# Kernel optimization log

Measured on AMD Instinct MI355X. Metric: run time of the kernel, lower is better.

## Reference

```python
import jax, jax.numpy as jnp
import numpy as np

H = 512   # hidden_size
E = 256   # embedding_size
V = 32000 # vocab_size
L = 1024  # max_length (encoder seq len)
B = 64    # batch


def setup_inputs() -> dict:
    key = jax.random.key(0)
    ks = jax.random.split(key, 18)
    n = lambda i, shape, s=0.05: (jax.random.normal(ks[i], shape, dtype=jnp.float32) * s)
    return {
        "input": jax.random.randint(ks[0], (B, 1), 0, V),
        "last_output_context": n(1, (1, B, H), 1.0),
        "last_hidden": n(2, (1, B, H), 1.0),
        "last_cell_state": n(3, (1, B, H), 1.0),
        "encoder_outputs": n(4, (L, B, H), 1.0),
        "emb": n(5, (V, E)),
        "W_ih": n(6, (4 * H, E + H)),
        "W_hh": n(7, (4 * H, H)),
        "b_ih": n(8, (4 * H,)),
        "b_hh": n(9, (4 * H,)),
        "W_attn": n(10, (H, 2 * H)),
        "b_attn": n(11, (H,)),
        "beta": n(12, (H, 1), 1.0),
        "W_oc": n(13, (H, 2 * H)),
        "b_oc": n(14, (H,)),
        "W_out": n(15, (V, H)),
        "b_out": n(16, (V,)),
    }


def reference(input, last_output_context, last_hidden, last_cell_state,
              encoder_outputs, emb, W_ih, W_hh, b_ih, b_hh,
              W_attn, b_attn, beta, W_oc, b_oc, W_out, b_out):
    # embedding lookup: (B,1) -> (B,E)  (permute(1,0,2) then squeeze step dim)
    tok = emb[input[:, 0]]                                   # (B, E)
    x = jnp.concatenate([tok, last_output_context[0]], axis=1)  # (B, E+H)
    # single-step LSTM (PyTorch gate order i, f, g, o)
    gates = x @ W_ih.T + last_hidden[0] @ W_hh.T + b_ih + b_hh  # (B, 4H)
    i_g, f_g, g_g, o_g = jnp.split(gates, 4, axis=1)
    i_g = jax.nn.sigmoid(i_g)
    f_g = jax.nn.sigmoid(f_g)
    g_g = jnp.tanh(g_g)
    o_g = jax.nn.sigmoid(o_g)
    c = f_g * last_cell_state[0] + i_g * g_g                  # (B, H)
    h = o_g * jnp.tanh(c)                                     # (B, H) == rnn_output
    # additive attention, vectorized over the seq_len loop
    h_tiled = jnp.broadcast_to(h[None], (L, B, H))
    cat = jnp.concatenate([h_tiled, encoder_outputs], axis=-1)  # (L, B, 2H)
    energy = jnp.tanh(cat @ W_attn.T + b_attn) @ beta           # (L, B, 1)
    attn_w = jax.nn.softmax(energy[..., 0], axis=0)             # (L, B) softmax over seq
    # context = bmm(attn_weights, encoder_outputs)
    context = jnp.einsum('lb,lbh->bh', attn_w, encoder_outputs)  # (B, H)
    co = jnp.tanh(jnp.concatenate([h, context], axis=1) @ W_oc.T + b_oc)  # (B, H)
    output = jax.nn.log_softmax(co @ W_out.T + b_out, axis=1)    # (B, V)
    return output, co[None], h[None], c[None]
```

## Files before the change

kernel.cpp:

```cpp
#include <hip/hip_runtime.h>
#include <hip/hip_bf16.h>
#include <cstddef>

#define H   512
#define E   256
#define V   32000
#define L   1024
#define B   64
#define KX  768
#define M_TOT 65536

typedef __attribute__((ext_vector_type(8))) _Float16 half8v;
typedef __attribute__((ext_vector_type(4))) float f32x4;

__device__ __forceinline__ half8v cvt8(float4 x0, float4 x1) {
    union { half8v v; _Float16 u[8]; } hv;
    hv.u[0] = (_Float16)x0.x; hv.u[1] = (_Float16)x0.y;
    hv.u[2] = (_Float16)x0.z; hv.u[3] = (_Float16)x0.w;
    hv.u[4] = (_Float16)x1.x; hv.u[5] = (_Float16)x1.y;
    hv.u[6] = (_Float16)x1.z; hv.u[7] = (_Float16)x1.w;
    return hv.v;
}

__device__ __forceinline__ void glds16(const void* g, void* l) {
    __builtin_amdgcn_global_load_lds(
        (const __attribute__((address_space(1))) void*)g,
        (__attribute__((address_space(3))) void*)l, 16, 0, 0);
}

__global__ __launch_bounds__(256) void k_conv_w3(const float* __restrict__ W_attn,
                                                 unsigned short* __restrict__ WfB) {
    int u = blockIdx.x * 256 + threadIdx.x;
    int lane = u & 63;
    int rest = u >> 6;
    int kh = rest & 1, nf = (rest >> 1) & 3, wn = (rest >> 3) & 1;
    int kt2 = (rest >> 4) & 7, jt = rest >> 7;
    int j = jt * 128 + wn * 64 + nf * 16 + (lane & 15);
    int col = kt2 * 64 + kh * 32 + (lane >> 4) * 8;
    const float* src = &W_attn[(size_t)j * (2 * H) + H + col];
    float4 x0 = *reinterpret_cast<const float4*>(src);
    float4 x1 = *reinterpret_cast<const float4*>(src + 4);
    *reinterpret_cast<half8v*>(&WfB[(size_t)u * 8]) = cvt8(x0, x1);
}

__global__ __launch_bounds__(256) void k_build(const int* __restrict__ inp,
                                               const float* __restrict__ loc,
                                               const float* __restrict__ hprev,
                                               const float* __restrict__ emb,
                                               float* __restrict__ xprevT) {
    int gid = blockIdx.x * 256 + threadIdx.x;
    int k = gid >> 6, b = gid & 63;
    float v;
    if (k < 256)      v = emb[(size_t)inp[b] * E + k];
    else if (k < 768) v = loc[b * H + (k - 256)];
    else              v = hprev[b * H + (k - 768)];
    xprevT[gid] = v;
}

__global__ __launch_bounds__(256) void k_lstm(const float* __restrict__ W_ih,
                                              const float* __restrict__ W_hh,
                                              const float* __restrict__ b_ih,
                                              const float* __restrict__ b_hh,
                                              const float* __restrict__ xprevT,
                                              const float* __restrict__ cprev,
                                              float* __restrict__ h_out,
                                              float* __restrict__ c_out,
                                              float* __restrict__ hnewT) {
    int u = blockIdx.x;
    int w = threadIdx.x >> 6;
    int b = threadIdx.x & 63;
    int j = w * 512 + u;
    float a0 = 0.f, a1 = 0.f, a2 = 0.f, a3 = 0.f;
    const float* Wr = &W_ih[(size_t)j * KX];
    for (int k = 0; k < KX; k += 4) {
        float4 wv = *reinterpret_cast<const float4*>(&Wr[k]);
        a0 += wv.x * xprevT[(k + 0) * 64 + b];
        a1 += wv.y * xprevT[(k + 1) * 64 + b];
        a2 += wv.z * xprevT[(k + 2) * 64 + b];
        a3 += wv.w * xprevT[(k + 3) * 64 + b];
    }
    const float* Wr2 = &W_hh[(size_t)j * H];
    const float* hT = &xprevT[KX * 64];
    for (int k = 0; k < H; k += 4) {
        float4 wv = *reinterpret_cast<const float4*>(&Wr2[k]);
        a0 += wv.x * hT[(k + 0) * 64 + b];
        a1 += wv.y * hT[(k + 1) * 64 + b];
        a2 += wv.z * hT[(k + 2) * 64 + b];
        a3 += wv.w * hT[(k + 3) * 64 + b];
    }
    float acc = b_ih[j] + b_hh[j] + ((a0 + a1) + (a2 + a3));
    __shared__ float gs[4][64];
    gs[w][b] = acc;
    __syncthreads();
    if (threadIdx.x < 64) {
        float ig = 1.f / (1.f + __expf(-gs[0][b]));
        float fg = 1.f / (1.f + __expf(-gs[1][b]));
        float gg = tanhf(gs[2][b]);
        float og = 1.f / (1.f + __expf(-gs[3][b]));
        float c = fg * cprev[b * H + u] + ig * gg;
        float h = og * tanhf(c);
        c_out[b * H + u] = c;
        h_out[b * H + u] = h;
        hnewT[u * 64 + b] = h;
    }
}

__global__ __launch_bounds__(256) void k_hw(const float* __restrict__ W_attn,
                                            const float* __restrict__ b_attn,
                                            const float* __restrict__ hT,
                                            float* __restrict__ hW_jb) {
    int j = blockIdx.x * 4 + (threadIdx.x >> 6);
    int b = threadIdx.x & 63;
    float a0 = 0.f, a1 = 0.f, a2 = 0.f, a3 = 0.f;
    const float* Wr = &W_attn[(size_t)j * (2 * H)];
    for (int k = 0; k < H; k += 4) {
        float4 wv = *reinterpret_cast<const float4*>(&Wr[k]);
        a0 += wv.x * hT[(k + 0) * 64 + b];
        a1 += wv.y * hT[(k + 1) * 64 + b];
        a2 += wv.z * hT[(k + 2) * 64 + b];
        a3 += wv.w * hT[(k + 3) * 64 + b];
    }
    hW_jb[j * 64 + b] = b_attn[j] + ((a0 + a1) + (a2 + a3));
}

__global__ __launch_bounds__(256, 3) void k_energy_v11(
        const float* __restrict__ enc,
        const unsigned short* __restrict__ WfB,
        const float* __restrict__ hW,
        const float* __restrict__ beta,
        float* __restrict__ partial_e) {
    __shared__ float Af[8192];
    __shared__ unsigned short Bh[8192];
    __shared__ float red[2][128];

    const int tid  = threadIdx.x;
    const int lane = tid & 63;
    const int w    = tid >> 6;
    const int wm = w >> 1;
    const int wn = w & 1;
    const int bid = blockIdx.x;
    const int xcd = bid & 7;
    const int loc = bid >> 3;
    const int mt  = xcd * 64 + (loc >> 2);
    const int jt  = loc & 3;
    const int m0 = mt * 128;
    const int j0 = jt * 128;

    const int fr = lane & 15;
    const int g  = lane >> 4;

    const float* asrc[8];
    #pragma unroll
    for (int i = 0; i < 8; ++i) {
        int idx2 = w * 8 + i;
        int q  = idx2 >> 2;
        int kh = (idx2 >> 1) & 1;
        int c  = idx2 & 1;
        int row = q * 16 + fr;
        int col = kh * 32 + g * 8 + c * 4;
        asrc[i] = enc + (size_t)(m0 + row) * H + col;
    }
    const unsigned short* bsrc = WfB + (size_t)jt * 65536
                               + ((size_t)(w * 4) * 64 + lane) * 8;

    f32x4 acc[4][4];
    #pragma unroll
    for (int i = 0; i < 4; ++i)
        #pragma unroll
        for (int j = 0; j < 4; ++j) acc[i][j] = (f32x4){0.f, 0.f, 0.f, 0.f};

    for (int kt2 = 0; kt2 < 8; ++kt2) {
        #pragma unroll
        for (int i = 0; i < 8; ++i)
            glds16(asrc[i] + kt2 * 64, &Af[(w * 8 + i) * 256 + lane * 4]);
        #pragma unroll
        for (int i = 0; i < 4; ++i)
            glds16(bsrc + (size_t)kt2 * 8192 + i * 512,
                   &Bh[((w * 4 + i) * 64 + lane) * 8]);
        __syncthreads();
        #pragma unroll
        for (int kh = 0; kh < 2; ++kh) {
            half8v a_h[4], b_h[4];
            #pragma unroll
            for (int mf = 0; mf < 4; ++mf) {
                int q = wm * 4 + mf;
                int cb = ((q * 2 + kh) * 2) * 256 + lane * 4;
                float4 f0 = *reinterpret_cast<const float4*>(&Af[cb]);
                float4 f1 = *reinterpret_cast<const float4*>(&Af[cb + 256]);
                a_h[mf] = cvt8(f0, f1);
            }
            #pragma unroll
            for (int nf = 0; nf < 4; ++nf) {
                int cb = (((wn * 4 + nf) * 2 + kh) * 64 + lane) * 8;
                b_h[nf] = *reinterpret_cast<const half8v*>(&Bh[cb]);
            }
            #pragma unroll
            for (int mf = 0; mf < 4; ++mf)
                #pragma unroll
                for (int nf = 0; nf < 4; ++nf)
                    acc[mf][nf] = __builtin_amdgcn_mfma_f32_16x16x32_f16(
                        a_h[mf], b_h[nf], acc[mf][nf], 0, 0, 0);
        }
        __syncthreads();
    }

    float psum[4][4];
    #pragma unroll
    for (int i = 0; i < 4; ++i)
        #pragma unroll
        for (int r = 0; r < 4; ++r) psum[i][r] = 0.f;
    #pragma unroll
    for (int nf = 0; nf < 4; ++nf) {
        int jj = j0 + wn * 64 + nf * 16 + (lane & 15);
        float bet = beta[jj];
        #pragma unroll
        for (int mf = 0; mf < 4; ++mf) {
            int b_base = (wm * 64 + mf * 16 + (lane >> 4) * 4) & 63;
            float4 hw4 = *reinterpret_cast<const float4*>(&hW[jj * 64 + b_base]);
            float hwv[4] = {hw4.x, hw4.y, hw4.z, hw4.w};
            #pragma unroll
            for (int r = 0; r < 4; ++r) {
                float e = acc[mf][nf][r] + hwv[r];
                float ex = __expf(2.f * e);
                psum[mf][r] += bet * (1.f - 2.f / (ex + 1.f));
            }
        }
    }
    #pragma unroll
    for (int mf = 0; mf < 4; ++mf)
        #pragma unroll
        for (int r = 0; r < 4; ++r) {
            float v = psum[mf][r];
            v += __shfl_xor(v, 1);
            v += __shfl_xor(v, 2);
            v += __shfl_xor(v, 4);
            v += __shfl_xor(v, 8);
            psum[mf][r] = v;
        }
    __syncthreads();
    if ((lane & 15) == 0) {
        #pragma unroll
        for (int mf = 0; mf < 4; ++mf)
            #pragma unroll
            for (int r = 0; r < 4; ++r)
                red[wn][wm * 64 + mf * 16 + (lane >> 4) * 4 + r] = psum[mf][r];
    }
    __syncthreads();
    if (tid < 128)
        partial_e[(size_t)jt * M_TOT + m0 + tid] = red[0][tid] + red[1][tid];
}

__global__ __launch_bounds__(256) void k_softmax_l(const float* __restrict__ partial_e,
                                                   float* __restrict__ attn_w) {
    int b = blockIdx.x;
    int tid = threadIdx.x;
    float el[4];
    float m = -1e30f;
    #pragma unroll
    for (int i = 0; i < 4; ++i) {
        int l = i * 256 + tid;
        float e = 0.f;
        #pragma unroll
        for (int nb = 0; nb < 4; ++nb)
            e += partial_e[(size_t)nb * M_TOT + l * 64 + b];
        el[i] = e;
        m = fmaxf(m, e);
    }
    #pragma unroll
    for (int s = 1; s < 64; s <<= 1) m = fmaxf(m, __shfl_xor(m, s));
    __shared__ float redm[4];
    if ((tid & 63) == 0) redm[tid >> 6] = m;
    __syncthreads();
    m = fmaxf(fmaxf(redm[0], redm[1]), fmaxf(redm[2], redm[3]));
    float s = 0.f;
    #pragma unroll
    for (int i = 0; i < 4; ++i) { el[i] = __expf(el[i] - m); s += el[i]; }
    #pragma unroll
    for (int sh = 1; sh < 64; sh <<= 1) s += __shfl_xor(s, sh);
    __shared__ float reds[4];
    if ((tid & 63) == 0) reds[tid >> 6] = s;
    __syncthreads();
    s = reds[0] + reds[1] + reds[2] + reds[3];
    float inv = 1.f / s;
    #pragma unroll
    for (int i = 0; i < 4; ++i)
        attn_w[(i * 256 + tid) * 64 + b] = el[i] * inv;
}

__global__ __launch_bounds__(128) void k_ctx_part(const float* __restrict__ attn_w,
                                                  const float* __restrict__ enc,
                                                  float* __restrict__ ctx_part) {
    int chunk = blockIdx.x, b = blockIdx.y;
    int h = threadIdx.x * 4;
    float4 acc = {0.f, 0.f, 0.f, 0.f};
    for (int i = 0; i < 32; ++i) {
        int l = chunk * 32 + i;
        float w = attn_w[l * 64 + b];
        float4 e4 = *reinterpret_cast<const float4*>(
            &enc[((size_t)l * 64 + b) * H + h]);
        acc.x += w * e4.x;
        acc.y += w * e4.y;
        acc.z += w * e4.z;
        acc.w += w * e4.w;
    }
    *reinterpret_cast<float4*>(&ctx_part[((size_t)(chunk * 64 + b)) * H + h]) = acc;
}

__global__ __launch_bounds__(256) void k_ctx_reduce(const float* __restrict__ ctx_part,
                                                    float* __restrict__ ctxT) {
    int gid = blockIdx.x * 256 + threadIdx.x;
    int b = gid >> 9, h = gid & 511;
    float s = 0.f;
    for (int c = 0; c < 32; ++c)
        s += ctx_part[((size_t)(c * 64 + b)) * H + h];
    ctxT[h * 64 + b] = s;
}

__global__ __launch_bounds__(256) void k_co(const float* __restrict__ W_oc,
                                            const float* __restrict__ b_oc,
                                            const float* __restrict__ hT,
                                            const float* __restrict__ ctxT,
                                            float* __restrict__ co_out) {
    int j = blockIdx.x * 4 + (threadIdx.x >> 6);
    int b = threadIdx.x & 63;
    float a0 = 0.f, a1 = 0.f, a2 = 0.f, a3 = 0.f;
    const float* Wr = &W_oc[(size_t)j * (2 * H)];
    for (int k = 0; k < H; k += 4) {
        float4 wv = *reinterpret_cast<const float4*>(&Wr[k]);
        a0 += wv.x * hT[(k + 0) * 64 + b];
        a1 += wv.y * hT[(k + 1) * 64 + b];
        a2 += wv.z * hT[(k + 2) * 64 + b];
        a3 += wv.w * hT[(k + 3) * 64 + b];
    }
    const float* Wr2 = Wr + H;
    for (int k = 0; k < H; k += 4) {
        float4 wv = *reinterpret_cast<const float4*>(&Wr2[k]);
        a0 += wv.x * ctxT[(k + 0) * 64 + b];
        a1 += wv.y * ctxT[(k + 1) * 64 + b];
        a2 += wv.z * ctxT[(k + 2) * 64 + b];
        a3 += wv.w * ctxT[(k + 3) * 64 + b];
    }
    co_out[b * H + j] = tanhf(b_oc[j] + ((a0 + a1) + (a2 + a3)));
}

__global__ __launch_bounds__(256) void k_logits_v3(const float* __restrict__ co,
                                                   const float* __restrict__ W_out,
                                                   const float* __restrict__ b_out,
                                                   float* __restrict__ logits) {
    const int tid  = threadIdx.x;
    const int lane = tid & 63;
    const int w    = tid >> 6;
    const int fr   = lane & 15;
    const int kb   = (lane >> 4) * 8;
    const int j    = blockIdx.x * 64 + w * 16 + fr;

    f32x4 acc[4];
    #pragma unroll
    for (int mf = 0; mf < 4; ++mf) acc[mf] = (f32x4){0.f, 0.f, 0.f, 0.f};

    const float* Arow = &co[(size_t)fr * H + kb];
    const float* Brow = &W_out[(size_t)j * H + kb];

    for (int k0 = 0; k0 < H; k0 += 32) {
        float4 b0 = *reinterpret_cast<const float4*>(Brow + k0);
        float4 b1 = *reinterpret_cast<const float4*>(Brow + k0 + 4);
        half8v bh = cvt8(b0, b1);
        #pragma unroll
        for (int mf = 0; mf < 4; ++mf) {
            const float* ap = Arow + (size_t)mf * 16 * H + k0;
            float4 a0 = *reinterpret_cast<const float4*>(ap);
            float4 a1 = *reinterpret_cast<const float4*>(ap + 4);
            half8v ah = cvt8(a0, a1);
            acc[mf] = __builtin_amdgcn_mfma_f32_16x16x32_f16(ah, bh, acc[mf], 0, 0, 0);
        }
    }
    float bo = b_out[j];
    #pragma unroll
    for (int mf = 0; mf < 4; ++mf) {
        int mbase = mf * 16 + (lane >> 4) * 4;
        #pragma unroll
        for (int r = 0; r < 4; ++r)
            logits[(size_t)(mbase + r) * V + j] = acc[mf][r] + bo;
    }
}

__global__ __launch_bounds__(256) void k_lsm_part(const float* __restrict__ logits,
                                                  float* __restrict__ pmax,
                                                  float* __restrict__ psum) {
    int chunk = blockIdx.x, b = blockIdx.y;
    int tid = threadIdx.x;
    const float* row = &logits[(size_t)b * V + chunk * 4000];
    float v[16];
    float m = -1e30f;
    #pragma unroll
    for (int t = 0; t < 16; ++t) {
        int i = t * 256 + tid;
        v[t] = (i < 4000) ? row[i] : -1e30f;
        m = fmaxf(m, v[t]);
    }
    #pragma unroll
    for (int s = 1; s < 64; s <<= 1) m = fmaxf(m, __shfl_xor(m, s));
    __shared__ float redm[4];
    if ((tid & 63) == 0) redm[tid >> 6] = m;
    __syncthreads();
    m = fmaxf(fmaxf(redm[0], redm[1]), fmaxf(redm[2], redm[3]));
    float s = 0.f;
    #pragma unroll
    for (int t = 0; t < 16; ++t) s += __expf(v[t] - m);
    #pragma unroll
    for (int sh = 1; sh < 64; sh <<= 1) s += __shfl_xor(s, sh);
    __shared__ float reds[4];
    if ((tid & 63) == 0) reds[tid >> 6] = s;
    __syncthreads();
    if (tid == 0) {
        pmax[chunk * 64 + b] = m;
        psum[chunk * 64 + b] = reds[0] + reds[1] + reds[2] + reds[3];
    }
}

__global__ __launch_bounds__(64) void k_lsm_final(const float* __restrict__ pmax,
                                                  const float* __restrict__ psum,
                                                  float* __restrict__ lse) {
    int b = threadIdx.x;
    float m = -1e30f;
    #pragma unroll
    for (int c = 0; c < 8; ++c) m = fmaxf(m, pmax[c * 64 + b]);
    float s = 0.f;
    #pragma unroll
    for (int c = 0; c < 8; ++c) s += psum[c * 64 + b] * __expf(pmax[c * 64 + b] - m);
    lse[b] = m + __logf(s);
}

__global__ __launch_bounds__(256) void k_lsm_write(const float* __restrict__ logits,
                                                   const float* __restrict__ lse,
                                                   float* __restrict__ out) {
    size_t i4 = ((size_t)blockIdx.x * 256 + threadIdx.x) * 4;
    int b = (int)(i4 / V);
    float l = lse[b];
    float4 x = *reinterpret_cast<const float4*>(&logits[i4]);
    x.x -= l; x.y -= l; x.z -= l; x.w -= l;
    *reinterpret_cast<float4*>(&out[i4]) = x;
}

extern "C" void kernel_launch(void* const* d_in, const int* in_sizes, int n_in,
                              void* d_out, int out_size, void* d_ws, size_t ws_size,
                              hipStream_t stream) {
    const int*   inp    = (const int*)  d_in[0];
    const float* loc    = (const float*)d_in[1];
    const float* hprev  = (const float*)d_in[2];
    const float* cprev  = (const float*)d_in[3];
    const float* enc    = (const float*)d_in[4];
    const float* emb    = (const float*)d_in[5];
    const float* W_ih   = (const float*)d_in[6];
    const float* W_hh   = (const float*)d_in[7];
    const float* b_ih   = (const float*)d_in[8];
    const float* b_hh   = (const float*)d_in[9];
    const float* W_attn = (const float*)d_in[10];
    const float* b_attn = (const float*)d_in[11];
    const float* beta   = (const float*)d_in[12];
    const float* W_oc   = (const float*)d_in[13];
    const float* b_oc   = (const float*)d_in[14];
    const float* W_out  = (const float*)d_in[15];
    const float* b_out  = (const float*)d_in[16];

    float* out = (float*)d_out;
    float* out_co = out + (size_t)B * V;
    float* out_h  = out_co + B * H;
    float* out_c  = out_h  + B * H;

    float* ws = (float*)d_ws;
    float* xprevT = ws;
    float* hnewT  = xprevT + 1280 * 64;
    float* hW     = hnewT  + H * 64;
    float* pe     = hW     + H * 64;
    float* attnw  = pe     + 4 * M_TOT;
    float* ctxp   = attnw  + M_TOT;
    float* ctxT   = ctxp   + 32 * 64 * H;
    float* logits = ctxT   + H * 64;
    float* pmax   = logits + (size_t)B * V;
    float* psum   = pmax   + 512;
    float* lse    = psum   + 512;
    unsigned short* WfB = (unsigned short*)(lse + 64);

    k_conv_w3<<<128, 256, 0, stream>>>(W_attn, WfB);
    k_build <<<320, 256, 0, stream>>>(inp, loc, hprev, emb, xprevT);
    k_lstm  <<<512, 256, 0, stream>>>(W_ih, W_hh, b_ih, b_hh, xprevT, cprev,
                                      out_h, out_c, hnewT);
    k_hw    <<<128, 256, 0, stream>>>(W_attn, b_attn, hnewT, hW);
    k_energy_v11<<<2048, 256, 0, stream>>>(enc, WfB, hW, beta, pe);
    k_softmax_l<<<64, 256, 0, stream>>>(pe, attnw);
    k_ctx_part <<<dim3(32, 64), 128, 0, stream>>>(attnw, enc, ctxp);
    k_ctx_reduce<<<128, 256, 0, stream>>>(ctxp, ctxT);
    k_co    <<<128, 256, 0, stream>>>(W_oc, b_oc, hnewT, ctxT, out_co);
    k_logits_v3<<<500, 256, 0, stream>>>(out_co, W_out, b_out, logits);
    k_lsm_part<<<dim3(8, 64), 256, 0, stream>>>(logits, pmax, psum);
    k_lsm_final<<<1, 64, 0, stream>>>(pmax, psum, lse);
    k_lsm_write<<<2000, 256, 0, stream>>>(logits, lse, out);
}
```

Measured before the change: 284.4 us.

## Halve energy GEMM K-tile with XOR-swizzled LDS, fuse prep and lsm_final kernels

Result: faster. 254.3 us, median of 2 (-10.6%).

```diff
diff --git a/kernel.cpp b/kernel.cpp
--- a/kernel.cpp
+++ b/kernel.cpp
@@ -28,33 +28,36 @@
         (__attribute__((address_space(3))) void*)l, 16, 0, 0);
 }
 
-__global__ __launch_bounds__(256) void k_conv_w3(const float* __restrict__ W_attn,
-                                                 unsigned short* __restrict__ WfB) {
-    int u = blockIdx.x * 256 + threadIdx.x;
-    int lane = u & 63;
-    int rest = u >> 6;
-    int kh = rest & 1, nf = (rest >> 1) & 3, wn = (rest >> 3) & 1;
-    int kt2 = (rest >> 4) & 7, jt = rest >> 7;
-    int j = jt * 128 + wn * 64 + nf * 16 + (lane & 15);
-    int col = kt2 * 64 + kh * 32 + (lane >> 4) * 8;
-    const float* src = &W_attn[(size_t)j * (2 * H) + H + col];
-    float4 x0 = *reinterpret_cast<const float4*>(src);
-    float4 x1 = *reinterpret_cast<const float4*>(src + 4);
-    *reinterpret_cast<half8v*>(&WfB[(size_t)u * 8]) = cvt8(x0, x1);
-}
-
-__global__ __launch_bounds__(256) void k_build(const int* __restrict__ inp,
-                                               const float* __restrict__ loc,
-                                               const float* __restrict__ hprev,
-                                               const float* __restrict__ emb,
-                                               float* __restrict__ xprevT) {
-    int gid = blockIdx.x * 256 + threadIdx.x;
-    int k = gid >> 6, b = gid & 63;
-    float v;
-    if (k < 256)      v = emb[(size_t)inp[b] * E + k];
-    else if (k < 768) v = loc[b * H + (k - 256)];
-    else              v = hprev[b * H + (k - 768)];
-    xprevT[gid] = v;
+__global__ __launch_bounds__(256) void k_prep(const float* __restrict__ W_attn,
+                                              unsigned short* __restrict__ WfB,
+                                              const int* __restrict__ inp,
+                                              const float* __restrict__ loc,
+                                              const float* __restrict__ hprev,
+                                              const float* __restrict__ emb,
+                                              float* __restrict__ xprevT) {
+    if (blockIdx.x < 128) {
+        int u = blockIdx.x * 256 + threadIdx.x;
+        int lane = u & 63;
+        int rest = u >> 6;
+        int f = rest & 7;
+        int kt = (rest >> 3) & 15;
+        int jt = rest >> 7;
+        int wn = f >> 2, nf = f & 3;
+        int j = jt * 128 + wn * 64 + nf * 16 + (lane & 15);
+        int col = kt * 32 + (lane >> 4) * 8;
+        const float* src = &W_attn[(size_t)j * (2 * H) + H + col];
+        float4 x0 = *reinterpret_cast<const float4*>(src);
+        float4 x1 = *reinterpret_cast<const float4*>(src + 4);
+        *reinterpret_cast<half8v*>(&WfB[(size_t)u * 8]) = cvt8(x0, x1);
+    } else {
+        int gid = (blockIdx.x - 128) * 256 + threadIdx.x;
+        int k = gid >> 6, b = gid & 63;
+        float v;
+        if (k < 256)      v = emb[(size_t)inp[b] * E + k];
+        else if (k < 768) v = loc[b * H + (k - 256)];
+        else              v = hprev[b * H + (k - 768)];
+        xprevT[gid] = v;
+    }
 }
 
 __global__ __launch_bounds__(256) void k_lstm(const float* __restrict__ W_ih,
@@ -123,14 +126,14 @@
     hW_jb[j * 64 + b] = b_attn[j] + ((a0 + a1) + (a2 + a3));
 }
 
-__global__ __launch_bounds__(256, 3) void k_energy_v11(
+__global__ __launch_bounds__(256, 4) void k_energy_v12(
         const float* __restrict__ enc,
         const unsigned short* __restrict__ WfB,
         const float* __restrict__ hW,
         const float* __restrict__ beta,
         float* __restrict__ partial_e) {
-    __shared__ float Af[8192];
-    __shared__ unsigned short Bh[8192];
+    __shared__ float Af[4096];
+    __shared__ unsigned short Bh2[4096];
     __shared__ float red[2][128];
 
     const int tid  = threadIdx.x;
@@ -149,19 +152,15 @@
     const int fr = lane & 15;
     const int g  = lane >> 4;
 
-    const float* asrc[8];
-    #pragma unroll
-    for (int i = 0; i < 8; ++i) {
-        int idx2 = w * 8 + i;
-        int q  = idx2 >> 2;
-        int kh = (idx2 >> 1) & 1;
-        int c  = idx2 & 1;
-        int row = q * 16 + fr;
-        int col = kh * 32 + g * 8 + c * 4;
-        asrc[i] = enc + (size_t)(m0 + row) * H + col;
-    }
-    const unsigned short* bsrc = WfB + (size_t)jt * 65536
-                               + ((size_t)(w * 4) * 64 + lane) * 8;
+    const float* asrcA[4];
+    #pragma unroll
+    for (int i = 0; i < 4; ++i) {
+        int c0 = (w * 4 + i) * 64 + lane;
+        int row = c0 >> 3;
+        int sc = (lane & 7) ^ (row & 7);
+        asrcA[i] = enc + (size_t)(m0 + row) * H + sc * 4;
+    }
+    const size_t bbase = (size_t)jt * 16 * 512;
 
     f32x4 acc[4][4];
     #pragma unroll
@@ -169,38 +168,35 @@
         #pragma unroll
         for (int j = 0; j < 4; ++j) acc[i][j] = (f32x4){0.f, 0.f, 0.f, 0.f};
 
-    for (int kt2 = 0; kt2 < 8; ++kt2) {
-        #pragma unroll
-        for (int i = 0; i < 8; ++i)
-            glds16(asrc[i] + kt2 * 64, &Af[(w * 8 + i) * 256 + lane * 4]);
+    for (int kt = 0; kt < 16; ++kt) {
         #pragma unroll
         for (int i = 0; i < 4; ++i)
-            glds16(bsrc + (size_t)kt2 * 8192 + i * 512,
-                   &Bh[((w * 4 + i) * 64 + lane) * 8]);
+            glds16(asrcA[i] + kt * 32, &Af[((w * 4 + i) * 64 + lane) * 4]);
+        #pragma unroll
+        for (int i = 0; i < 2; ++i)
+            glds16(WfB + (bbase + (size_t)kt * 512 + (w * 2 + i) * 64 + lane) * 8,
+                   &Bh2[((w * 2 + i) * 64 + lane) * 8]);
         __syncthreads();
-        #pragma unroll
-        for (int kh = 0; kh < 2; ++kh) {
-            half8v a_h[4], b_h[4];
+        half8v a_h[4], b_h[4];
+        #pragma unroll
+        for (int mf = 0; mf < 4; ++mf) {
+            int R = wm * 64 + mf * 16 + fr;
+            int p0 = (2 * g) ^ (R & 7);
+            int p1 = p0 ^ 1;
+            float4 f0 = *reinterpret_cast<const float4*>(&Af[(R * 8 + p0) * 4]);
+            float4 f1 = *reinterpret_cast<const float4*>(&Af[(R * 8 + p1) * 4]);
+            a_h[mf] = cvt8(f0, f1);
+        }
+        #pragma unroll
+        for (int nf = 0; nf < 4; ++nf)
+            b_h[nf] = *reinterpret_cast<const half8v*>(
+                &Bh2[((wn * 4 + nf) * 64 + lane) * 8]);
+        #pragma unroll
+        for (int mf = 0; mf < 4; ++mf)
             #pragma unroll
-            for (int mf = 0; mf < 4; ++mf) {
-                int q = wm * 4 + mf;
-                int cb = ((q * 2 + kh) * 2) * 256 + lane * 4;
-                float4 f0 = *reinterpret_cast<const float4*>(&Af[cb]);
-                float4 f1 = *reinterpret_cast<const float4*>(&Af[cb + 256]);
-                a_h[mf] = cvt8(f0, f1);
-            }
-            #pragma unroll
-            for (int nf = 0; nf < 4; ++nf) {
-                int cb = (((wn * 4 + nf) * 2 + kh) * 64 + lane) * 8;
-                b_h[nf] = *reinterpret_cast<const half8v*>(&Bh[cb]);
-            }
-            #pragma unroll
-            for (int mf = 0; mf < 4; ++mf)
-                #pragma unroll
-                for (int nf = 0; nf < 4; ++nf)
-                    acc[mf][nf] = __builtin_amdgcn_mfma_f32_16x16x32_f16(
-                        a_h[mf], b_h[nf], acc[mf][nf], 0, 0, 0);
-        }
+            for (int nf = 0; nf < 4; ++nf)
+                acc[mf][nf] = __builtin_amdgcn_mfma_f32_16x16x32_f16(
+                    a_h[mf], b_h[nf], acc[mf][nf], 0, 0, 0);
         __syncthreads();
     }
 
@@ -418,25 +414,19 @@
     }
 }
 
-__global__ __launch_bounds__(64) void k_lsm_final(const float* __restrict__ pmax,
-                                                  const float* __restrict__ psum,
-                                                  float* __restrict__ lse) {
-    int b = threadIdx.x;
-    float m = -1e30f;
-    #pragma unroll
-    for (int c = 0; c < 8; ++c) m = fmaxf(m, pmax[c * 64 + b]);
-    float s = 0.f;
-    #pragma unroll
-    for (int c = 0; c < 8; ++c) s += psum[c * 64 + b] * __expf(pmax[c * 64 + b] - m);
-    lse[b] = m + __logf(s);
-}
-
 __global__ __launch_bounds__(256) void k_lsm_write(const float* __restrict__ logits,
-                                                   const float* __restrict__ lse,
+                                                   const float* __restrict__ pmax,
+                                                   const float* __restrict__ psum,
                                                    float* __restrict__ out) {
     size_t i4 = ((size_t)blockIdx.x * 256 + threadIdx.x) * 4;
     int b = (int)(i4 / V);
-    float l = lse[b];
+    float m = -1e30f;
+    #pragma unroll
+    for (int c = 0; c < 8; ++c) m = fmaxf(m, pmax[c * 64 + b]);
+    float s = 0.f;
+    #pragma unroll
+    for (int c = 0; c < 8; ++c) s += psum[c * 64 + b] * __expf(pmax[c * 64 + b] - m);
+    float l = m + __logf(s);
     float4 x = *reinterpret_cast<const float4*>(&logits[i4]);
     x.x -= l; x.y -= l; x.z -= l; x.w -= l;
     *reinterpret_cast<float4*>(&out[i4]) = x;
@@ -482,18 +472,16 @@
     float* lse    = psum   + 512;
     unsigned short* WfB = (unsigned short*)(lse + 64);
 
-    k_conv_w3<<<128, 256, 0, stream>>>(W_attn, WfB);
-    k_build <<<320, 256, 0, stream>>>(inp, loc, hprev, emb, xprevT);
+    k_prep  <<<448, 256, 0, stream>>>(W_attn, WfB, inp, loc, hprev, emb, xprevT);
     k_lstm  <<<512, 256, 0, stream>>>(W_ih, W_hh, b_ih, b_hh, xprevT, cprev,
                                       out_h, out_c, hnewT);
     k_hw    <<<128, 256, 0, stream>>>(W_attn, b_attn, hnewT, hW);
-    k_energy_v11<<<2048, 256, 0, stream>>>(enc, WfB, hW, beta, pe);
+    k_energy_v12<<<2048, 256, 0, stream>>>(enc, WfB, hW, beta, pe);
     k_softmax_l<<<64, 256, 0, stream>>>(pe, attnw);
     k_ctx_part <<<dim3(32, 64), 128, 0, stream>>>(attnw, enc, ctxp);
     k_ctx_reduce<<<128, 256, 0, stream>>>(ctxp, ctxT);
     k_co    <<<128, 256, 0, stream>>>(W_oc, b_oc, hnewT, ctxT, out_co);
     k_logits_v3<<<500, 256, 0, stream>>>(out_co, W_out, b_out, logits);
     k_lsm_part<<<dim3(8, 64), 256, 0, stream>>>(logits, pmax, psum);
-    k_lsm_final<<<1, 64, 0, stream>>>(pmax, psum, lse);
-    k_lsm_write<<<2000, 256, 0, stream>>>(logits, lse, out);
-}
+    k_lsm_write<<<2000, 256, 0, stream>>>(logits, pmax, psum, out);
+}
```
